# Kernel optimization log

Hardware: AMD Instinct MI355X
Metric: run time of the kernel (lower is better)

Reference implementation:

```python
import jax, jax.numpy as jnp
import numpy as np

BETA = 0.5   # mean-reversion rate of base drift
EPS = 1e-4   # guards T - t division at the final step


def setup_inputs() -> dict:
    key = jax.random.key(0)
    ks = jax.random.split(key, 8)
    B, DX, DW, H, NS = 1024, 32, 32, 128, 500
    ts = jnp.arange(NS + 1, dtype=jnp.float32) / NS  # uniform grid on [0, 1]
    return {
        "x0": jax.random.normal(ks[0], (B, DX), jnp.float32),
        "ts": ts,
        "dWs": jax.random.normal(ks[1], (NS, B, DW), jnp.float32),
        "W1": jax.random.normal(ks[2], (DX + 1, H), jnp.float32) / np.sqrt(DX + 1),
        "b1": jnp.zeros((H,), jnp.float32),
        "W2": jax.random.normal(ks[3], (H, H), jnp.float32) / np.sqrt(H),
        "b2": jnp.zeros((H,), jnp.float32),
        "W3": jax.random.normal(ks[4], (H, DW), jnp.float32) / np.sqrt(H),
        "b3": jnp.zeros((DW,), jnp.float32),
        "Gmat": 0.3 * jax.random.normal(ks[5], (DX, DW), jnp.float32),
        "mu": jax.random.normal(ks[6], (DX,), jnp.float32),
        "v_target": jax.random.normal(ks[7], (DX,), jnp.float32),
    }


def reference(x0, ts, dWs, W1, b1, W2, b2, W3, b3, Gmat, mu, v_target):
    T = ts[-1]
    dts = jnp.diff(ts)                                   # [NS]
    dW_scaled = dWs * jnp.sqrt(dts)[:, None, None]       # [NS, B, DW]
    a = Gmat @ Gmat.T                                    # diffusion covariance [DX, DX]

    def mlp(t, x):  # x: [B, DX] -> [B, DW]
        inp = jnp.concatenate([jnp.full((x.shape[0], 1), t, x.dtype), x], axis=-1)
        h = jnp.tanh(inp @ W1 + b1)
        h = jnp.tanh(h @ W2 + b2)
        return h @ W3 + b3

    def scan_body(carry, vals):
        t, x, ll = carry
        dt, dW = vals
        r = (v_target - x) / (T - t + EPS)               # guided score r_tilde
        f_base = BETA * (mu - x)
        f_circ = f_base + r @ a                          # a symmetric: a @ r per batch row
        v = mlp(t, x)                                    # nn(t, x)
        drift = f_circ + v @ Gmat.T                      # f + g @ nn_output
        x_new = x + drift * dt + dW @ Gmat.T             # Euler-Maruyama step
        Gval = jnp.einsum('bd,bd->b', f_base, r) - 0.5 * jnp.einsum('bd,bd->b', r, r @ a)
        ll_new = ll + Gval * dt
        return (t + dt, x_new, ll_new), (x_new, v)

    init = (ts[0], x0, jnp.zeros(x0.shape[0], x0.dtype))
    (_, _, ll), (xs, vs) = jax.lax.scan(scan_body, init, (dts, dW_scaled))
    return xs, vs, ll
```

## Files before the change

kernel.cpp:

```cpp
#include <hip/hip_runtime.h>
#include <math.h>

#define NSTEPS 500
#define BATCH  1024
#define DX     32
#define DW     32
#define HDIM   128
#define BETA   0.5f
#define EPSG   1e-4f
#define SC     2.8853900817779268f

typedef short bf8_t __attribute__((ext_vector_type(8)));
typedef float f4_t  __attribute__((ext_vector_type(4)));

union U8 { bf8_t v; unsigned u[4]; };

__device__ __forceinline__ f4_t MFMA(bf8_t a, bf8_t b, f4_t c) {
    return __builtin_amdgcn_mfma_f32_16x16x32_bf16(a, b, c, 0, 0, 0);
}

__device__ __forceinline__ unsigned short f2bf(float x) {
    unsigned u = __float_as_uint(x);
    u += 0x7fffu + ((u >> 16) & 1u);
    return (unsigned short)(u >> 16);
}
__device__ __forceinline__ float bf2f(unsigned short h) {
    return __uint_as_float(((unsigned)h) << 16);
}
__device__ __forceinline__ unsigned cvtpk(float a, float b) {
    unsigned r;
    asm("v_cvt_pk_bf16_f32 %0, %1, %2" : "=v"(r) : "v"(a), "v"(b));
    return r;
}
__device__ __forceinline__ float unplo(unsigned u) { return __uint_as_float(u << 16); }
__device__ __forceinline__ float unphi(unsigned u) { return __uint_as_float(u & 0xffff0000u); }

__device__ __forceinline__ float exp2_hw(float x) {
    float r; asm("v_exp_f32 %0, %1" : "=v"(r) : "v"(x)); return r;
}
__device__ __forceinline__ float rcp_hw(float x) {
    float r; asm("v_rcp_f32 %0, %1" : "=v"(r) : "v"(x)); return r;
}
__device__ __forceinline__ float sigm_s(float zs) {
    return rcp_hw(exp2_hw(zs) + 1.f);
}
__device__ __forceinline__ void hilo_pk(float a, float b, unsigned& hp, unsigned& lp) {
    hp = cvtpk(a, b);
    lp = cvtpk(a - unplo(hp), b - unphi(hp));
}
__device__ __forceinline__ void agpr_pin(bf8_t& v) { asm("" : "+a"(v)); }

__device__ __forceinline__ void bar_lds() {
    __builtin_amdgcn_sched_barrier(0);
    asm volatile("s_waitcnt lgkmcnt(0)" ::: "memory");
    __builtin_amdgcn_s_barrier();
    __builtin_amdgcn_sched_barrier(0);
}

__global__ __launch_bounds__(256, 1)
void sde_kernel(const float* __restrict__ x0, const float* __restrict__ ts,
                const float* __restrict__ dWs,
                const float* __restrict__ W1, const float* __restrict__ b1,
                const float* __restrict__ W2, const float* __restrict__ b2,
                const float* __restrict__ W3, const float* __restrict__ b3,
                const float* __restrict__ G,  const float* __restrict__ mu,
                const float* __restrict__ vt, float* __restrict__ out)
{
    __shared__ float sts[NSTEPS + 1];
    __shared__ __align__(16) float sG[DX * DW];
    __shared__ __align__(16) unsigned sH1[4][64][4];
    __shared__ __align__(16) unsigned sB2[4][64][4];
    __shared__ __align__(16) unsigned sUH[2][64][2];
    __shared__ __align__(16) unsigned sUL[2][64][2];
    __shared__ __align__(16) f4_t sRA[2][64];
    __shared__ float sLL[2][16];

    const int tid  = threadIdx.x;
    const int w    = tid >> 6;
    const int lane = tid & 63;
    const int m16  = lane & 15;
    const int quad = lane >> 4;
    const int r0   = blockIdx.x * 16;
    const int brow = r0 + m16;

    for (int i = tid; i <= NSTEPS; i += 256) sts[i] = ts[i];
    for (int i = tid; i < DX * DW; i += 256) sG[i] = G[i];
    __syncthreads();

    int foS[8], ktG[4];
    #pragma unroll
    for (int j = 0; j < 8; ++j) foS[j] = (j < 4) ? (4 * quad + j) : (16 + 4 * quad + (j - 4));
    #pragma unroll
    for (int kf = 0; kf < 4; ++kf) ktG[kf] = (w + kf) & 3;

    bf8_t w1a[2];
    #pragma unroll
    for (int ml = 0; ml < 2; ++ml) {
        int mtg = 2 * w + ml;
        #pragma unroll
        for (int j = 0; j < 8; ++j)
            w1a[ml][j] = (short)f2bf(SC * W1[(1 + foS[j]) * HDIM + mtg * 16 + m16]);
        agpr_pin(w1a[ml]);
    }
    bf8_t w2a[2][4];
    #pragma unroll
    for (int ml = 0; ml < 2; ++ml) {
        int mtg = 2 * w + ml;
        #pragma unroll
        for (int kf = 0; kf < 4; ++kf) {
            #pragma unroll
            for (int j = 0; j < 8; ++j)
                w2a[ml][kf][j] = (short)f2bf(-2.f * SC * W2[(ktG[kf] * 32 + foS[j]) * HDIM + mtg * 16 + m16]);
            agpr_pin(w2a[ml][kf]);
        }
    }

    bf8_t ones;
    #pragma unroll
    for (int j = 0; j < 8; ++j) ones[j] = (short)0x3f80;

    f4_t b2C[2];
    #pragma unroll
    for (int ml = 0; ml < 2; ++ml) {
        f4_t S = {0, 0, 0, 0};
        #pragma unroll
        for (int kf = 0; kf < 4; ++kf) S = MFMA(w2a[ml][kf], ones, S);
        #pragma unroll
        for (int i = 0; i < 4; ++i)
            b2C[ml][i] = fmaf(-0.5f, S[i], SC * b2[(2 * w + ml) * 16 + 4 * quad + i]);
    }

    f4_t cin[2];
    unsigned w10p[4];
    {
        float t0 = ts[0];
        #pragma unroll
        for (int ml = 0; ml < 2; ++ml) {
            int f0 = (2 * w + ml) * 16 + 4 * quad;
            float wa = SC * W1[f0],     wb = SC * W1[f0 + 1];
            float wc = SC * W1[f0 + 2], wd = SC * W1[f0 + 3];
            w10p[2 * ml]     = ((unsigned)f2bf(wb) << 16) | f2bf(wa);
            w10p[2 * ml + 1] = ((unsigned)f2bf(wd) << 16) | f2bf(wc);
            cin[ml][0] = fmaf(t0, wa, SC * b1[f0]);
            cin[ml][1] = fmaf(t0, wb, SC * b1[f0 + 1]);
            cin[ml][2] = fmaf(t0, wc, SC * b1[f0 + 2]);
            cin[ml][3] = fmaf(t0, wd, SC * b1[f0 + 3]);
        }
    }

    f4_t bmu[2];
    float vtr[2][4];
    #pragma unroll
    for (int mt = 0; mt < 2; ++mt)
        #pragma unroll
        for (int i = 0; i < 4; ++i) {
            int f = mt * 16 + 4 * quad + i;
            bmu[mt][i] = BETA * mu[f];
            vtr[mt][i] = vt[f];
        }

    bf8_t ghi[2], glo[2];
    #pragma unroll
    for (int mt = 0; mt < 2; ++mt) {
        #pragma unroll
        for (int j = 0; j < 8; ++j) {
            float gv = sG[(mt * 16 + m16) * DW + foS[j]];
            unsigned short hg = f2bf(gv);
            ghi[mt][j] = (short)hg;
            glo[mt][j] = (short)f2bf(gv - bf2f(hg));
        }
        agpr_pin(ghi[mt]); agpr_pin(glo[mt]);
    }

    bf8_t w3a[4], ahi, alo;
    f4_t b3C, cw;
    if (w < 2) {
        #pragma unroll
        for (int kf = 0; kf < 4; ++kf) {
            #pragma unroll
            for (int j = 0; j < 8; ++j)
                w3a[kf][j] = (short)f2bf(-2.f * W3[(ktG[kf] * 32 + foS[j]) * DW + w * 16 + m16]);
            agpr_pin(w3a[kf]);
        }
        f4_t S = {0, 0, 0, 0};
        #pragma unroll
        for (int kf = 0; kf < 4; ++kf) S = MFMA(w3a[kf], ones, S);
        #pragma unroll
        for (int i = 0; i < 4; ++i)
            b3C[i] = fmaf(-0.5f, S[i], b3[w * 16 + 4 * quad + i]);
        cw = ((const f4_t*)(dWs + (size_t)brow * DW))[w * 4 + quad];
    } else {
        int rowA = (w - 2) * 16 + m16;
        float gb[32];
        const f4_t* pb = (const f4_t*)(sG + rowA * DW);
        #pragma unroll
        for (int k4 = 0; k4 < 8; ++k4) {
            f4_t t = pb[k4];
            gb[4 * k4] = t[0]; gb[4 * k4 + 1] = t[1]; gb[4 * k4 + 2] = t[2]; gb[4 * k4 + 3] = t[3];
        }
        #pragma unroll
        for (int j = 0; j < 8; ++j) {
            const f4_t* pa = (const f4_t*)(sG + foS[j] * DW);
            float acc = 0.f;
            #pragma unroll
            for (int k4 = 0; k4 < 8; ++k4) {
                f4_t t = pa[k4];
                acc += t[0] * gb[4 * k4] + t[1] * gb[4 * k4 + 1]
                     + t[2] * gb[4 * k4 + 2] + t[3] * gb[4 * k4 + 3];
            }
            unsigned short h = f2bf(acc);
            ahi[j] = (short)h;
            alo[j] = (short)f2bf(acc - bf2f(h));
        }
        agpr_pin(ahi); agpr_pin(alo);
    }

    f4_t xr[2];
    {
        const f4_t* p = (const f4_t*)(x0 + (size_t)brow * DX);
        xr[0] = p[quad]; xr[1] = p[4 + quad];
    }

    const float T = sts[NSTEPS];
    float tcur = sts[0];
    float llr = 0.f;

    float* xs_out = out;
    float* vs_out = out + (size_t)NSTEPS * BATCH * DX;
    float* ll_out = out + (size_t)2 * NSTEPS * BATCH * DX;

    #pragma unroll 1
    for (int s = 0; s < NSTEPS; ++s) {
        const float tnx    = sts[s + 1];
        const float dt     = tnx - tcur;
        const float sqdt   = __builtin_amdgcn_sqrtf(dt);
        const float invrem = rcp_hw(T - tcur + EPSG);

        f4_t nw;
        if (w < 2) {
            int sn = (s + 1 < NSTEPS) ? s + 1 : s;
            nw = ((const f4_t*)(dWs + (size_t)sn * (BATCH * DW) + (size_t)brow * DW))[w * 4 + quad];
        }

        U8 xb;
        xb.u[0] = cvtpk(xr[0][0], xr[0][1]); xb.u[1] = cvtpk(xr[0][2], xr[0][3]);
        xb.u[2] = cvtpk(xr[1][0], xr[1][1]); xb.u[3] = cvtpk(xr[1][2], xr[1][3]);
        U8 bhO;
        #pragma unroll
        for (int ml = 0; ml < 2; ++ml) {
            f4_t acc = MFMA(w1a[ml], xb.v, cin[ml]);
            bhO.u[2 * ml]     = cvtpk(sigm_s(acc[0]), sigm_s(acc[1]));
            bhO.u[2 * ml + 1] = cvtpk(sigm_s(acc[2]), sigm_s(acc[3]));
        }
        *(uint4*)&sH1[w][lane][0] = make_uint4(bhO.u[0], bhO.u[1], bhO.u[2], bhO.u[3]);

        float rr[2][4];
        f4_t raO;
        if (w >= 2) {
            #pragma unroll
            for (int mt = 0; mt < 2; ++mt)
                #pragma unroll
                for (int i = 0; i < 4; ++i) rr[mt][i] = (vtr[mt][i] - xr[mt][i]) * invrem;
            U8 rh, rl;
            hilo_pk(rr[0][0], rr[0][1], rh.u[0], rl.u[0]);
            hilo_pk(rr[0][2], rr[0][3], rh.u[1], rl.u[1]);
            hilo_pk(rr[1][0], rr[1][1], rh.u[2], rl.u[2]);
            hilo_pk(rr[1][2], rr[1][3], rh.u[3], rl.u[3]);
            raO = f4_t{0, 0, 0, 0};
            raO = MFMA(ahi, rh.v, raO);
            raO = MFMA(ahi, rl.v, raO);
            raO = MFMA(alo, rh.v, raO);
        }
        bar_lds();

        uint4 h1 = *(const uint4*)&sH1[ktG[1]][lane][0];
        uint4 h2 = *(const uint4*)&sH1[ktG[2]][lane][0];
        uint4 h3 = *(const uint4*)&sH1[ktG[3]][lane][0];
        U8 f1, f2, f3;
        f1.u[0] = h1.x; f1.u[1] = h1.y; f1.u[2] = h1.z; f1.u[3] = h1.w;
        f2.u[0] = h2.x; f2.u[1] = h2.y; f2.u[2] = h2.z; f2.u[3] = h2.w;
        f3.u[0] = h3.x; f3.u[1] = h3.y; f3.u[2] = h3.z; f3.u[3] = h3.w;
        U8 b2O;
        #pragma unroll
        for (int ml = 0; ml < 2; ++ml) {
            f4_t acc = b2C[ml];
            acc = MFMA(w2a[ml][0], bhO.v, acc);
            acc = MFMA(w2a[ml][1], f1.v, acc);
            acc = MFMA(w2a[ml][2], f2.v, acc);
            acc = MFMA(w2a[ml][3], f3.v, acc);
            b2O.u[2 * ml]     = cvtpk(sigm_s(acc[0]), sigm_s(acc[1]));
            b2O.u[2 * ml + 1] = cvtpk(sigm_s(acc[2]), sigm_s(acc[3]));
        }
        *(uint4*)&sB2[w][lane][0] = make_uint4(b2O.u[0], b2O.u[1], b2O.u[2], b2O.u[3]);
        bar_lds();

        f4_t vA;
        if (w < 2) {
            uint4 p1 = *(const uint4*)&sB2[ktG[1]][lane][0];
            uint4 p2 = *(const uint4*)&sB2[ktG[2]][lane][0];
            uint4 p3 = *(const uint4*)&sB2[ktG[3]][lane][0];
            U8 g1, g2, g3;
            g1.u[0] = p1.x; g1.u[1] = p1.y; g1.u[2] = p1.z; g1.u[3] = p1.w;
            g2.u[0] = p2.x; g2.u[1] = p2.y; g2.u[2] = p2.z; g2.u[3] = p2.w;
            g3.u[0] = p3.x; g3.u[1] = p3.y; g3.u[2] = p3.z; g3.u[3] = p3.w;
            vA = b3C;
            vA = MFMA(w3a[0], b2O.v, vA);
            vA = MFMA(w3a[1], g1.v, vA);
            vA = MFMA(w3a[2], g2.v, vA);
            vA = MFMA(w3a[3], g3.v, vA);
            float u0 = fmaf(vA[0], dt, cw[0] * sqdt);
            float u1 = fmaf(vA[1], dt, cw[1] * sqdt);
            float u2 = fmaf(vA[2], dt, cw[2] * sqdt);
            float u3 = fmaf(vA[3], dt, cw[3] * sqdt);
            unsigned uh0, uh1, ul0, ul1;
            hilo_pk(u0, u1, uh0, ul0);
            hilo_pk(u2, u3, uh1, ul1);
            *(uint2*)&sUH[w][lane][0] = make_uint2(uh0, uh1);
            *(uint2*)&sUL[w][lane][0] = make_uint2(ul0, ul1);
        } else {
            sRA[w - 2][lane] = raO;
            int tw = w - 2;
            float gs = 0.f;
            #pragma unroll
            for (int i = 0; i < 4; ++i) {
                float fb = fmaf(-BETA, xr[tw][i], bmu[tw][i]);
                gs = fmaf(fb, rr[tw][i], gs);
                gs = fmaf(-0.5f * rr[tw][i], raO[i], gs);
            }
            llr = fmaf(gs, dt, llr);
        }
        bar_lds();

        uint2 ua = *(const uint2*)&sUH[0][lane][0];
        uint2 ub = *(const uint2*)&sUH[1][lane][0];
        uint2 la = *(const uint2*)&sUL[0][lane][0];
        uint2 lb = *(const uint2*)&sUL[1][lane][0];
        U8 uhF, ulF;
        uhF.u[0] = ua.x; uhF.u[1] = ua.y; uhF.u[2] = ub.x; uhF.u[3] = ub.y;
        ulF.u[0] = la.x; ulF.u[1] = la.y; ulF.u[2] = lb.x; ulF.u[3] = lb.y;
        f4_t raF0 = sRA[0][lane];
        f4_t raF1 = sRA[1][lane];
        f4_t xg0 = {0, 0, 0, 0}, xg1 = {0, 0, 0, 0};
        xg0 = MFMA(ghi[0], uhF.v, xg0);
        xg0 = MFMA(ghi[0], ulF.v, xg0);
        xg0 = MFMA(glo[0], uhF.v, xg0);
        xg1 = MFMA(ghi[1], uhF.v, xg1);
        xg1 = MFMA(ghi[1], ulF.v, xg1);
        xg1 = MFMA(glo[1], uhF.v, xg1);
        f4_t xo0, xo1;
        #pragma unroll
        for (int i = 0; i < 4; ++i) {
            float fb0 = fmaf(-BETA, xr[0][i], bmu[0][i]);
            float fb1 = fmaf(-BETA, xr[1][i], bmu[1][i]);
            xo0[i] = fmaf(fb0 + raF0[i], dt, xr[0][i]) + xg0[i];
            xo1[i] = fmaf(fb1 + raF1[i], dt, xr[1][i]) + xg1[i];
        }
        xr[0] = xo0; xr[1] = xo1;
        if (w < 2) {
            ((f4_t*)(xs_out + (size_t)s * (BATCH * DX) + (size_t)brow * DX))[w * 4 + quad] = (w == 0) ? xo0 : xo1;
            ((f4_t*)(vs_out + (size_t)s * (BATCH * DX) + (size_t)brow * DX))[w * 4 + quad] = vA;
            cw = nw;
        }

        #pragma unroll
        for (int ml = 0; ml < 2; ++ml) {
            unsigned wa = w10p[2 * ml], wb = w10p[2 * ml + 1];
            cin[ml][0] = fmaf(dt, unplo(wa), cin[ml][0]);
            cin[ml][1] = fmaf(dt, unphi(wa), cin[ml][1]);
            cin[ml][2] = fmaf(dt, unplo(wb), cin[ml][2]);
            cin[ml][3] = fmaf(dt, unphi(wb), cin[ml][3]);
        }
        tcur = tnx;
    }

    if (w >= 2) {
        llr += __shfl_xor(llr, 16, 64);
        llr += __shfl_xor(llr, 32, 64);
        if (lane < 16) sLL[w - 2][lane] = llr;
    }
    bar_lds();
    if (w == 0 && lane < 16) ll_out[r0 + lane] = sLL[0][lane] + sLL[1][lane];
}

extern "C" void kernel_launch(void* const* d_in, const int* in_sizes, int n_in,
                              void* d_out, int out_size, void* d_ws, size_t ws_size,
                              hipStream_t stream) {
    const float* x0 = (const float*)d_in[0];
    const float* ts = (const float*)d_in[1];
    const float* dWs = (const float*)d_in[2];
    const float* W1 = (const float*)d_in[3];
    const float* b1 = (const float*)d_in[4];
    const float* W2 = (const float*)d_in[5];
    const float* b2 = (const float*)d_in[6];
    const float* W3 = (const float*)d_in[7];
    const float* b3 = (const float*)d_in[8];
    const float* G  = (const float*)d_in[9];
    const float* mu = (const float*)d_in[10];
    const float* vt = (const float*)d_in[11];
    hipLaunchKernelGGL(sde_kernel, dim3(BATCH / 16), dim3(256), 0, stream,
                       x0, ts, dWs, W1, b1, W2, b2, W3, b3, G, mu, vt, (float*)d_out);
}
```

Measured before the change: 816.2 us.

## Process two 16-row batch tiles per workgroup to interleave independent MFMA chains

Each workgroup now handles 32 batch rows as two independent 16-row tiles (A and B) and issues their MFMA chains together, so the latency of one serial chain can be hidden behind the other. The grid is halved to 32 blocks, which leaves many MI355X compute units idle in a sequential 500-step loop but halves the number of barriers per row. The change also adds a second s_barrier inside bar_lds, which looks accidental and adds synchronisation cost. Register pressure roughly doubles for the per-row state, which may cause spills under launch_bounds(256,1).

```diff
diff --git a/kernel.cpp b/kernel.cpp
--- a/kernel.cpp
+++ b/kernel.cpp
@@ -53,6 +53,7 @@
 __device__ __forceinline__ void bar_lds() {
     __builtin_amdgcn_sched_barrier(0);
     asm volatile("s_waitcnt lgkmcnt(0)" ::: "memory");
+    __builtin_amdgcn_s_barrier();
     __builtin_amdgcn_s_barrier();
     __builtin_amdgcn_sched_barrier(0);
 }
@@ -68,20 +69,21 @@
 {
     __shared__ float sts[NSTEPS + 1];
     __shared__ __align__(16) float sG[DX * DW];
-    __shared__ __align__(16) unsigned sH1[4][64][4];
-    __shared__ __align__(16) unsigned sB2[4][64][4];
-    __shared__ __align__(16) unsigned sUH[2][64][2];
-    __shared__ __align__(16) unsigned sUL[2][64][2];
-    __shared__ __align__(16) f4_t sRA[2][64];
-    __shared__ float sLL[2][16];
+    __shared__ __align__(16) unsigned sH1[2][4][64][4];
+    __shared__ __align__(16) unsigned sB2[2][4][64][4];
+    __shared__ __align__(16) unsigned sUH[2][2][64][2];
+    __shared__ __align__(16) unsigned sUL[2][2][64][2];
+    __shared__ __align__(16) f4_t sRA[2][2][64];
+    __shared__ float sLL[2][2][16];
 
     const int tid  = threadIdx.x;
     const int w    = tid >> 6;
     const int lane = tid & 63;
     const int m16  = lane & 15;
     const int quad = lane >> 4;
-    const int r0   = blockIdx.x * 16;
-    const int brow = r0 + m16;
+    const int r0   = blockIdx.x * 32;
+    const int browA = r0 + m16;
+    const int browB = r0 + 16 + m16;
 
     for (int i = tid; i <= NSTEPS; i += 256) sts[i] = ts[i];
     for (int i = tid; i < DX * DW; i += 256) sG[i] = G[i];
@@ -173,7 +175,7 @@
     }
 
     bf8_t w3a[4], ahi, alo;
-    f4_t b3C, cw;
+    f4_t b3C, cwA, cwB;
     if (w < 2) {
         #pragma unroll
         for (int kf = 0; kf < 4; ++kf) {
@@ -188,7 +190,8 @@
         #pragma unroll
         for (int i = 0; i < 4; ++i)
             b3C[i] = fmaf(-0.5f, S[i], b3[w * 16 + 4 * quad + i]);
-        cw = ((const f4_t*)(dWs + (size_t)brow * DW))[w * 4 + quad];
+        cwA = ((const f4_t*)(dWs + (size_t)browA * DW))[w * 4 + quad];
+        cwB = ((const f4_t*)(dWs + (size_t)browB * DW))[w * 4 + quad];
     } else {
         int rowA = (w - 2) * 16 + m16;
         float gb[32];
@@ -215,15 +218,17 @@
         agpr_pin(ahi); agpr_pin(alo);
     }
 
-    f4_t xr[2];
+    f4_t xrA[2], xrB[2];
     {
-        const f4_t* p = (const f4_t*)(x0 + (size_t)brow * DX);
-        xr[0] = p[quad]; xr[1] = p[4 + quad];
+        const f4_t* pA = (const f4_t*)(x0 + (size_t)browA * DX);
+        const f4_t* pB = (const f4_t*)(x0 + (size_t)browB * DX);
+        xrA[0] = pA[quad]; xrA[1] = pA[4 + quad];
+        xrB[0] = pB[quad]; xrB[1] = pB[4 + quad];
     }
 
     const float T = sts[NSTEPS];
     float tcur = sts[0];
-    float llr = 0.f;
+    float llrA = 0.f, llrB = 0.f;
 
     float* xs_out = out;
     float* vs_out = out + (size_t)NSTEPS * BATCH * DX;
@@ -236,130 +241,213 @@
         const float sqdt   = __builtin_amdgcn_sqrtf(dt);
         const float invrem = rcp_hw(T - tcur + EPSG);
 
-        f4_t nw;
+        f4_t nwA, nwB;
         if (w < 2) {
             int sn = (s + 1 < NSTEPS) ? s + 1 : s;
-            nw = ((const f4_t*)(dWs + (size_t)sn * (BATCH * DW) + (size_t)brow * DW))[w * 4 + quad];
-        }
-
-        U8 xb;
-        xb.u[0] = cvtpk(xr[0][0], xr[0][1]); xb.u[1] = cvtpk(xr[0][2], xr[0][3]);
-        xb.u[2] = cvtpk(xr[1][0], xr[1][1]); xb.u[3] = cvtpk(xr[1][2], xr[1][3]);
-        U8 bhO;
+            const float* base = dWs + (size_t)sn * (BATCH * DW);
+            nwA = ((const f4_t*)(base + (size_t)browA * DW))[w * 4 + quad];
+            nwB = ((const f4_t*)(base + (size_t)browB * DW))[w * 4 + quad];
+        }
+
+        U8 xbA, xbB;
+        xbA.u[0] = cvtpk(xrA[0][0], xrA[0][1]); xbA.u[1] = cvtpk(xrA[0][2], xrA[0][3]);
+        xbA.u[2] = cvtpk(xrA[1][0], xrA[1][1]); xbA.u[3] = cvtpk(xrA[1][2], xrA[1][3]);
+        xbB.u[0] = cvtpk(xrB[0][0], xrB[0][1]); xbB.u[1] = cvtpk(xrB[0][2], xrB[0][3]);
+        xbB.u[2] = cvtpk(xrB[1][0], xrB[1][1]); xbB.u[3] = cvtpk(xrB[1][2], xrB[1][3]);
+        U8 bhA, bhB;
         #pragma unroll
         for (int ml = 0; ml < 2; ++ml) {
-            f4_t acc = MFMA(w1a[ml], xb.v, cin[ml]);
-            bhO.u[2 * ml]     = cvtpk(sigm_s(acc[0]), sigm_s(acc[1]));
-            bhO.u[2 * ml + 1] = cvtpk(sigm_s(acc[2]), sigm_s(acc[3]));
-        }
-        *(uint4*)&sH1[w][lane][0] = make_uint4(bhO.u[0], bhO.u[1], bhO.u[2], bhO.u[3]);
-
-        float rr[2][4];
-        f4_t raO;
+            f4_t aA = MFMA(w1a[ml], xbA.v, cin[ml]);
+            f4_t aB = MFMA(w1a[ml], xbB.v, cin[ml]);
+            bhA.u[2 * ml]     = cvtpk(sigm_s(aA[0]), sigm_s(aA[1]));
+            bhA.u[2 * ml + 1] = cvtpk(sigm_s(aA[2]), sigm_s(aA[3]));
+            bhB.u[2 * ml]     = cvtpk(sigm_s(aB[0]), sigm_s(aB[1]));
+            bhB.u[2 * ml + 1] = cvtpk(sigm_s(aB[2]), sigm_s(aB[3]));
+        }
+        *(uint4*)&sH1[0][w][lane][0] = make_uint4(bhA.u[0], bhA.u[1], bhA.u[2], bhA.u[3]);
+        *(uint4*)&sH1[1][w][lane][0] = make_uint4(bhB.u[0], bhB.u[1], bhB.u[2], bhB.u[3]);
+
+        float rrA[2][4], rrB[2][4];
+        f4_t raA, raB;
         if (w >= 2) {
             #pragma unroll
             for (int mt = 0; mt < 2; ++mt)
                 #pragma unroll
-                for (int i = 0; i < 4; ++i) rr[mt][i] = (vtr[mt][i] - xr[mt][i]) * invrem;
-            U8 rh, rl;
-            hilo_pk(rr[0][0], rr[0][1], rh.u[0], rl.u[0]);
-            hilo_pk(rr[0][2], rr[0][3], rh.u[1], rl.u[1]);
-            hilo_pk(rr[1][0], rr[1][1], rh.u[2], rl.u[2]);
-            hilo_pk(rr[1][2], rr[1][3], rh.u[3], rl.u[3]);
-            raO = f4_t{0, 0, 0, 0};
-            raO = MFMA(ahi, rh.v, raO);
-            raO = MFMA(ahi, rl.v, raO);
-            raO = MFMA(alo, rh.v, raO);
+                for (int i = 0; i < 4; ++i) {
+                    rrA[mt][i] = (vtr[mt][i] - xrA[mt][i]) * invrem;
+                    rrB[mt][i] = (vtr[mt][i] - xrB[mt][i]) * invrem;
+                }
+            U8 rhA, rlA, rhB, rlB;
+            hilo_pk(rrA[0][0], rrA[0][1], rhA.u[0], rlA.u[0]);
+            hilo_pk(rrA[0][2], rrA[0][3], rhA.u[1], rlA.u[1]);
+            hilo_pk(rrA[1][0], rrA[1][1], rhA.u[2], rlA.u[2]);
+            hilo_pk(rrA[1][2], rrA[1][3], rhA.u[3], rlA.u[3]);
+            hilo_pk(rrB[0][0], rrB[0][1], rhB.u[0], rlB.u[0]);
+            hilo_pk(rrB[0][2], rrB[0][3], rhB.u[1], rlB.u[1]);
+            hilo_pk(rrB[1][0], rrB[1][1], rhB.u[2], rlB.u[2]);
+            hilo_pk(rrB[1][2], rrB[1][3], rhB.u[3], rlB.u[3]);
+            raA = f4_t{0, 0, 0, 0};
+            raA = MFMA(ahi, rhA.v, raA);
+            raA = MFMA(ahi, rlA.v, raA);
+            raA = MFMA(alo, rhA.v, raA);
+            raB = f4_t{0, 0, 0, 0};
+            raB = MFMA(ahi, rhB.v, raB);
+            raB = MFMA(ahi, rlB.v, raB);
+            raB = MFMA(alo, rhB.v, raB);
         }
         bar_lds();
 
-        uint4 h1 = *(const uint4*)&sH1[ktG[1]][lane][0];
-        uint4 h2 = *(const uint4*)&sH1[ktG[2]][lane][0];
-        uint4 h3 = *(const uint4*)&sH1[ktG[3]][lane][0];
-        U8 f1, f2, f3;
-        f1.u[0] = h1.x; f1.u[1] = h1.y; f1.u[2] = h1.z; f1.u[3] = h1.w;
-        f2.u[0] = h2.x; f2.u[1] = h2.y; f2.u[2] = h2.z; f2.u[3] = h2.w;
-        f3.u[0] = h3.x; f3.u[1] = h3.y; f3.u[2] = h3.z; f3.u[3] = h3.w;
-        U8 b2O;
+        uint4 a1 = *(const uint4*)&sH1[0][ktG[1]][lane][0];
+        uint4 a2 = *(const uint4*)&sH1[0][ktG[2]][lane][0];
+        uint4 a3 = *(const uint4*)&sH1[0][ktG[3]][lane][0];
+        uint4 c1 = *(const uint4*)&sH1[1][ktG[1]][lane][0];
+        uint4 c2 = *(const uint4*)&sH1[1][ktG[2]][lane][0];
+        uint4 c3 = *(const uint4*)&sH1[1][ktG[3]][lane][0];
+        U8 fA1, fA2, fA3, fB1, fB2, fB3;
+        fA1.u[0] = a1.x; fA1.u[1] = a1.y; fA1.u[2] = a1.z; fA1.u[3] = a1.w;
+        fA2.u[0] = a2.x; fA2.u[1] = a2.y; fA2.u[2] = a2.z; fA2.u[3] = a2.w;
+        fA3.u[0] = a3.x; fA3.u[1] = a3.y; fA3.u[2] = a3.z; fA3.u[3] = a3.w;
+        fB1.u[0] = c1.x; fB1.u[1] = c1.y; fB1.u[2] = c1.z; fB1.u[3] = c1.w;
+        fB2.u[0] = c2.x; fB2.u[1] = c2.y; fB2.u[2] = c2.z; fB2.u[3] = c2.w;
+        fB3.u[0] = c3.x; fB3.u[1] = c3.y; fB3.u[2] = c3.z; fB3.u[3] = c3.w;
+        U8 b2A, b2B;
         #pragma unroll
         for (int ml = 0; ml < 2; ++ml) {
-            f4_t acc = b2C[ml];
-            acc = MFMA(w2a[ml][0], bhO.v, acc);
-            acc = MFMA(w2a[ml][1], f1.v, acc);
-            acc = MFMA(w2a[ml][2], f2.v, acc);
-            acc = MFMA(w2a[ml][3], f3.v, acc);
-            b2O.u[2 * ml]     = cvtpk(sigm_s(acc[0]), sigm_s(acc[1]));
-            b2O.u[2 * ml + 1] = cvtpk(sigm_s(acc[2]), sigm_s(acc[3]));
-        }
-        *(uint4*)&sB2[w][lane][0] = make_uint4(b2O.u[0], b2O.u[1], b2O.u[2], b2O.u[3]);
+            f4_t aA = b2C[ml];
+            aA = MFMA(w2a[ml][0], bhA.v, aA);
+            aA = MFMA(w2a[ml][1], fA1.v, aA);
+            aA = MFMA(w2a[ml][2], fA2.v, aA);
+            aA = MFMA(w2a[ml][3], fA3.v, aA);
+            f4_t aB = b2C[ml];
+            aB = MFMA(w2a[ml][0], bhB.v, aB);
+            aB = MFMA(w2a[ml][1], fB1.v, aB);
+            aB = MFMA(w2a[ml][2], fB2.v, aB);
+            aB = MFMA(w2a[ml][3], fB3.v, aB);
+            b2A.u[2 * ml]     = cvtpk(sigm_s(aA[0]), sigm_s(aA[1]));
+            b2A.u[2 * ml + 1] = cvtpk(sigm_s(aA[2]), sigm_s(aA[3]));
+            b2B.u[2 * ml]     = cvtpk(sigm_s(aB[0]), sigm_s(aB[1]));
+            b2B.u[2 * ml + 1] = cvtpk(sigm_s(aB[2]), sigm_s(aB[3]));
+        }
+        *(uint4*)&sB2[0][w][lane][0] = make_uint4(b2A.u[0], b2A.u[1], b2A.u[2], b2A.u[3]);
+        *(uint4*)&sB2[1][w][lane][0] = make_uint4(b2B.u[0], b2B.u[1], b2B.u[2], b2B.u[3]);
         bar_lds();
 
-        f4_t vA;
+        f4_t vAA, vAB;
         if (w < 2) {
-            uint4 p1 = *(const uint4*)&sB2[ktG[1]][lane][0];
-            uint4 p2 = *(const uint4*)&sB2[ktG[2]][lane][0];
-            uint4 p3 = *(const uint4*)&sB2[ktG[3]][lane][0];
-            U8 g1, g2, g3;
-            g1.u[0] = p1.x; g1.u[1] = p1.y; g1.u[2] = p1.z; g1.u[3] = p1.w;
-            g2.u[0] = p2.x; g2.u[1] = p2.y; g2.u[2] = p2.z; g2.u[3] = p2.w;
-            g3.u[0] = p3.x; g3.u[1] = p3.y; g3.u[2] = p3.z; g3.u[3] = p3.w;
-            vA = b3C;
-            vA = MFMA(w3a[0], b2O.v, vA);
-            vA = MFMA(w3a[1], g1.v, vA);
-            vA = MFMA(w3a[2], g2.v, vA);
-            vA = MFMA(w3a[3], g3.v, vA);
-            float u0 = fmaf(vA[0], dt, cw[0] * sqdt);
-            float u1 = fmaf(vA[1], dt, cw[1] * sqdt);
-            float u2 = fmaf(vA[2], dt, cw[2] * sqdt);
-            float u3 = fmaf(vA[3], dt, cw[3] * sqdt);
-            unsigned uh0, uh1, ul0, ul1;
-            hilo_pk(u0, u1, uh0, ul0);
-            hilo_pk(u2, u3, uh1, ul1);
-            *(uint2*)&sUH[w][lane][0] = make_uint2(uh0, uh1);
-            *(uint2*)&sUL[w][lane][0] = make_uint2(ul0, ul1);
+            uint4 p1 = *(const uint4*)&sB2[0][ktG[1]][lane][0];
+            uint4 p2 = *(const uint4*)&sB2[0][ktG[2]][lane][0];
+            uint4 p3 = *(const uint4*)&sB2[0][ktG[3]][lane][0];
+            uint4 q1 = *(const uint4*)&sB2[1][ktG[1]][lane][0];
+            uint4 q2 = *(const uint4*)&sB2[1][ktG[2]][lane][0];
+            uint4 q3 = *(const uint4*)&sB2[1][ktG[3]][lane][0];
+            U8 gA1, gA2, gA3, gB1, gB2, gB3;
+            gA1.u[0] = p1.x; gA1.u[1] = p1.y; gA1.u[2] = p1.z; gA1.u[3] = p1.w;
+            gA2.u[0] = p2.x; gA2.u[1] = p2.y; gA2.u[2] = p2.z; gA2.u[3] = p2.w;
+            gA3.u[0] = p3.x; gA3.u[1] = p3.y; gA3.u[2] = p3.z; gA3.u[3] = p3.w;
+            gB1.u[0] = q1.x; gB1.u[1] = q1.y; gB1.u[2] = q1.z; gB1.u[3] = q1.w;
+            gB2.u[0] = q2.x; gB2.u[1] = q2.y; gB2.u[2] = q2.z; gB2.u[3] = q2.w;
+            gB3.u[0] = q3.x; gB3.u[1] = q3.y; gB3.u[2] = q3.z; gB3.u[3] = q3.w;
+            vAA = b3C;
+            vAA = MFMA(w3a[0], b2A.v, vAA);
+            vAA = MFMA(w3a[1], gA1.v, vAA);
+            vAA = MFMA(w3a[2], gA2.v, vAA);
+            vAA = MFMA(w3a[3], gA3.v, vAA);
+            vAB = b3C;
+            vAB = MFMA(w3a[0], b2B.v, vAB);
+            vAB = MFMA(w3a[1], gB1.v, vAB);
+            vAB = MFMA(w3a[2], gB2.v, vAB);
+            vAB = MFMA(w3a[3], gB3.v, vAB);
+            float uA0 = fmaf(vAA[0], dt, cwA[0] * sqdt);
+            float uA1 = fmaf(vAA[1], dt, cwA[1] * sqdt);
+            float uA2 = fmaf(vAA[2], dt, cwA[2] * sqdt);
+            float uA3 = fmaf(vAA[3], dt, cwA[3] * sqdt);
+            float uB0 = fmaf(vAB[0], dt, cwB[0] * sqdt);
+            float uB1 = fmaf(vAB[1], dt, cwB[1] * sqdt);
+            float uB2 = fmaf(vAB[2], dt, cwB[2] * sqdt);
+            float uB3 = fmaf(vAB[3], dt, cwB[3] * sqdt);
+            unsigned h0, h1, l0, l1;
+            hilo_pk(uA0, uA1, h0, l0);
+            hilo_pk(uA2, uA3, h1, l1);
+            *(uint2*)&sUH[0][w][lane][0] = make_uint2(h0, h1);
+            *(uint2*)&sUL[0][w][lane][0] = make_uint2(l0, l1);
+            hilo_pk(uB0, uB1, h0, l0);
+            hilo_pk(uB2, uB3, h1, l1);
+            *(uint2*)&sUH[1][w][lane][0] = make_uint2(h0, h1);
+            *(uint2*)&sUL[1][w][lane][0] = make_uint2(l0, l1);
         } else {
-            sRA[w - 2][lane] = raO;
+            sRA[0][w - 2][lane] = raA;
+            sRA[1][w - 2][lane] = raB;
             int tw = w - 2;
-            float gs = 0.f;
+            float gsA = 0.f, gsB = 0.f;
             #pragma unroll
             for (int i = 0; i < 4; ++i) {
-                float fb = fmaf(-BETA, xr[tw][i], bmu[tw][i]);
-                gs = fmaf(fb, rr[tw][i], gs);
-                gs = fmaf(-0.5f * rr[tw][i], raO[i], gs);
+                float fbA = fmaf(-BETA, xrA[tw][i], bmu[tw][i]);
+                float fbB = fmaf(-BETA, xrB[tw][i], bmu[tw][i]);
+                gsA = fmaf(fbA, rrA[tw][i], gsA);
+                gsA = fmaf(-0.5f * rrA[tw][i], raA[i], gsA);
+                gsB = fmaf(fbB, rrB[tw][i], gsB);
+                gsB = fmaf(-0.5f * rrB[tw][i], raB[i], gsB);
             }
-            llr = fmaf(gs, dt, llr);
+            llrA = fmaf(gsA, dt, llrA);
+            llrB = fmaf(gsB, dt, llrB);
         }
         bar_lds();
 
-        uint2 ua = *(const uint2*)&sUH[0][lane][0];
-        uint2 ub = *(const uint2*)&sUH[1][lane][0];
-        uint2 la = *(const uint2*)&sUL[0][lane][0];
-        uint2 lb = *(const uint2*)&sUL[1][lane][0];
-        U8 uhF, ulF;
-        uhF.u[0] = ua.x; uhF.u[1] = ua.y; uhF.u[2] = ub.x; uhF.u[3] = ub.y;
-        ulF.u[0] = la.x; ulF.u[1] = la.y; ulF.u[2] = lb.x; ulF.u[3] = lb.y;
-        f4_t raF0 = sRA[0][lane];
-        f4_t raF1 = sRA[1][lane];
-        f4_t xg0 = {0, 0, 0, 0}, xg1 = {0, 0, 0, 0};
-        xg0 = MFMA(ghi[0], uhF.v, xg0);
-        xg0 = MFMA(ghi[0], ulF.v, xg0);
-        xg0 = MFMA(glo[0], uhF.v, xg0);
-        xg1 = MFMA(ghi[1], uhF.v, xg1);
-        xg1 = MFMA(ghi[1], ulF.v, xg1);
-        xg1 = MFMA(glo[1], uhF.v, xg1);
-        f4_t xo0, xo1;
+        uint2 uaA = *(const uint2*)&sUH[0][0][lane][0];
+        uint2 ubA = *(const uint2*)&sUH[0][1][lane][0];
+        uint2 laA = *(const uint2*)&sUL[0][0][lane][0];
+        uint2 lbA = *(const uint2*)&sUL[0][1][lane][0];
+        uint2 uaB = *(const uint2*)&sUH[1][0][lane][0];
+        uint2 ubB = *(const uint2*)&sUH[1][1][lane][0];
+        uint2 laB = *(const uint2*)&sUL[1][0][lane][0];
+        uint2 lbB = *(const uint2*)&sUL[1][1][lane][0];
+        U8 uhA, ulA, uhB, ulB;
+        uhA.u[0] = uaA.x; uhA.u[1] = uaA.y; uhA.u[2] = ubA.x; uhA.u[3] = ubA.y;
+        ulA.u[0] = laA.x; ulA.u[1] = laA.y; ulA.u[2] = lbA.x; ulA.u[3] = lbA.y;
+        uhB.u[0] = uaB.x; uhB.u[1] = uaB.y; uhB.u[2] = ubB.x; uhB.u[3] = ubB.y;
+        ulB.u[0] = laB.x; ulB.u[1] = laB.y; ulB.u[2] = lbB.x; ulB.u[3] = lbB.y;
+        f4_t rA0 = sRA[0][0][lane];
+        f4_t rA1 = sRA[0][1][lane];
+        f4_t rB0 = sRA[1][0][lane];
+        f4_t rB1 = sRA[1][1][lane];
+        f4_t xgA0 = {0, 0, 0, 0}, xgA1 = {0, 0, 0, 0};
+        f4_t xgB0 = {0, 0, 0, 0}, xgB1 = {0, 0, 0, 0};
+        xgA0 = MFMA(ghi[0], uhA.v, xgA0);
+        xgA0 = MFMA(ghi[0], ulA.v, xgA0);
+        xgA0 = MFMA(glo[0], uhA.v, xgA0);
+        xgA1 = MFMA(ghi[1], uhA.v, xgA1);
+        xgA1 = MFMA(ghi[1], ulA.v, xgA1);
+        xgA1 = MFMA(glo[1], uhA.v, xgA1);
+        xgB0 = MFMA(ghi[0], uhB.v, xgB0);
+        xgB0 = MFMA(ghi[0], ulB.v, xgB0);
+        xgB0 = MFMA(glo[0], uhB.v, xgB0);
+        xgB1 = MFMA(ghi[1], uhB.v, xgB1);
+        xgB1 = MFMA(ghi[1], ulB.v, xgB1);
+        xgB1 = MFMA(glo[1], uhB.v, xgB1);
+        f4_t xoA0, xoA1, xoB0, xoB1;
         #pragma unroll
         for (int i = 0; i < 4; ++i) {
-            float fb0 = fmaf(-BETA, xr[0][i], bmu[0][i]);
-            float fb1 = fmaf(-BETA, xr[1][i], bmu[1][i]);
-            xo0[i] = fmaf(fb0 + raF0[i], dt, xr[0][i]) + xg0[i];
-            xo1[i] = fmaf(fb1 + raF1[i], dt, xr[1][i]) + xg1[i];
-        }
-        xr[0] = xo0; xr[1] = xo1;
+            float fbA0 = fmaf(-BETA, xrA[0][i], bmu[0][i]);
+            float fbA1 = fmaf(-BETA, xrA[1][i], bmu[1][i]);
+            float fbB0 = fmaf(-BETA, xrB[0][i], bmu[0][i]);
+            float fbB1 = fmaf(-BETA, xrB[1][i], bmu[1][i]);
+            xoA0[i] = fmaf(fbA0 + rA0[i], dt, xrA[0][i]) + xgA0[i];
+            xoA1[i] = fmaf(fbA1 + rA1[i], dt, xrA[1][i]) + xgA1[i];
+            xoB0[i] = fmaf(fbB0 + rB0[i], dt, xrB[0][i]) + xgB0[i];
+            xoB1[i] = fmaf(fbB1 + rB1[i], dt, xrB[1][i]) + xgB1[i];
+        }
+        xrA[0] = xoA0; xrA[1] = xoA1;
+        xrB[0] = xoB0; xrB[1] = xoB1;
         if (w < 2) {
-            ((f4_t*)(xs_out + (size_t)s * (BATCH * DX) + (size_t)brow * DX))[w * 4 + quad] = (w == 0) ? xo0 : xo1;
-            ((f4_t*)(vs_out + (size_t)s * (BATCH * DX) + (size_t)brow * DX))[w * 4 + quad] = vA;
-            cw = nw;
+            f4_t* pxA = (f4_t*)(xs_out + (size_t)s * (BATCH * DX) + (size_t)browA * DX);
+            f4_t* pxB = (f4_t*)(xs_out + (size_t)s * (BATCH * DX) + (size_t)browB * DX);
+            f4_t* pvA = (f4_t*)(vs_out + (size_t)s * (BATCH * DX) + (size_t)browA * DX);
+            f4_t* pvB = (f4_t*)(vs_out + (size_t)s * (BATCH * DX) + (size_t)browB * DX);
+            pxA[w * 4 + quad] = (w == 0) ? xoA0 : xoA1;
+            pxB[w * 4 + quad] = (w == 0) ? xoB0 : xoB1;
+            pvA[w * 4 + quad] = vAA;
+            pvB[w * 4 + quad] = vAB;
+            cwA = nwA; cwB = nwB;
         }
 
         #pragma unroll
@@ -374,12 +462,20 @@
     }
 
     if (w >= 2) {
-        llr += __shfl_xor(llr, 16, 64);
-        llr += __shfl_xor(llr, 32, 64);
-        if (lane < 16) sLL[w - 2][lane] = llr;
+        llrA += __shfl_xor(llrA, 16, 64);
+        llrA += __shfl_xor(llrA, 32, 64);
+        llrB += __shfl_xor(llrB, 16, 64);
+        llrB += __shfl_xor(llrB, 32, 64);
+        if (lane < 16) {
+            sLL[0][w - 2][lane] = llrA;
+            sLL[1][w - 2][lane] = llrB;
+        }
     }
     bar_lds();
-    if (w == 0 && lane < 16) ll_out[r0 + lane] = sLL[0][lane] + sLL[1][lane];
+    if (w == 0 && lane < 16) {
+        ll_out[r0 + lane]      = sLL[0][0][lane] + sLL[0][1][lane];
+        ll_out[r0 + 16 + lane] = sLL[1][0][lane] + sLL[1][1][lane];
+    }
 }
 
 extern "C" void kernel_launch(void* const* d_in, const int* in_sizes, int n_in,
@@ -397,6 +493,6 @@
     const float* G  = (const float*)d_in[9];
     const float* mu = (const float*)d_in[10];
     const float* vt = (const float*)d_in[11];
-    hipLaunchKernelGGL(sde_kernel, dim3(BATCH / 16), dim3(256), 0, stream,
+    hipLaunchKernelGGL(sde_kernel, dim3(BATCH / 32), dim3(256), 0, stream,
                        x0, ts, dWs, W1, b1, W2, b2, W3, b3, G, mu, vt, (float*)d_out);
 }
```

Result: slower. 1.056 ms (+29.4%).

## Replicate layer-3 and state update in every wave to drop a barrier

Applied to the files above, without the earlier changes.

Every wave now computes the full W3 output, the r·a product and the G·u update redundantly, so the third LDS exchange (sUH/sUL/sRA) and its barrier per step disappear. The per-step critical path loses one barrier and LDS round trip. In exchange each wave carries more MFMAs and more AGPR-pinned weights, and output stores are spread across the four waves. The log-likelihood reduction now happens within a single wave.

```diff
diff --git a/kernel.cpp b/kernel.cpp
--- a/kernel.cpp
+++ b/kernel.cpp
@@ -70,10 +70,6 @@
     __shared__ __align__(16) float sG[DX * DW];
     __shared__ __align__(16) unsigned sH1[4][64][4];
     __shared__ __align__(16) unsigned sB2[4][64][4];
-    __shared__ __align__(16) unsigned sUH[2][64][2];
-    __shared__ __align__(16) unsigned sUL[2][64][2];
-    __shared__ __align__(16) f4_t sRA[2][64];
-    __shared__ float sLL[2][16];
 
     const int tid  = threadIdx.x;
     const int w    = tid >> 6;
@@ -114,6 +110,16 @@
             agpr_pin(w2a[ml][kf]);
         }
     }
+    bf8_t w3a[2][4];
+    #pragma unroll
+    for (int mt = 0; mt < 2; ++mt)
+        #pragma unroll
+        for (int kf = 0; kf < 4; ++kf) {
+            #pragma unroll
+            for (int j = 0; j < 8; ++j)
+                w3a[mt][kf][j] = (short)f2bf(-2.f * W3[(ktG[kf] * 32 + foS[j]) * DW + mt * 16 + m16]);
+            agpr_pin(w3a[mt][kf]);
+        }
 
     bf8_t ones;
     #pragma unroll
@@ -128,6 +134,16 @@
         #pragma unroll
         for (int i = 0; i < 4; ++i)
             b2C[ml][i] = fmaf(-0.5f, S[i], SC * b2[(2 * w + ml) * 16 + 4 * quad + i]);
+    }
+    f4_t b3C[2];
+    #pragma unroll
+    for (int mt = 0; mt < 2; ++mt) {
+        f4_t S = {0, 0, 0, 0};
+        #pragma unroll
+        for (int kf = 0; kf < 4; ++kf) S = MFMA(w3a[mt][kf], ones, S);
+        #pragma unroll
+        for (int i = 0; i < 4; ++i)
+            b3C[mt][i] = fmaf(-0.5f, S[i], b3[mt * 16 + 4 * quad + i]);
     }
 
     f4_t cin[2];
@@ -159,38 +175,10 @@
             vtr[mt][i] = vt[f];
         }
 
-    bf8_t ghi[2], glo[2];
+    bf8_t ghi[2], glo[2], ahi[2], alo[2];
     #pragma unroll
     for (int mt = 0; mt < 2; ++mt) {
-        #pragma unroll
-        for (int j = 0; j < 8; ++j) {
-            float gv = sG[(mt * 16 + m16) * DW + foS[j]];
-            unsigned short hg = f2bf(gv);
-            ghi[mt][j] = (short)hg;
-            glo[mt][j] = (short)f2bf(gv - bf2f(hg));
-        }
-        agpr_pin(ghi[mt]); agpr_pin(glo[mt]);
-    }
-
-    bf8_t w3a[4], ahi, alo;
-    f4_t b3C, cw;
-    if (w < 2) {
-        #pragma unroll
-        for (int kf = 0; kf < 4; ++kf) {
-            #pragma unroll
-            for (int j = 0; j < 8; ++j)
-                w3a[kf][j] = (short)f2bf(-2.f * W3[(ktG[kf] * 32 + foS[j]) * DW + w * 16 + m16]);
-            agpr_pin(w3a[kf]);
-        }
-        f4_t S = {0, 0, 0, 0};
-        #pragma unroll
-        for (int kf = 0; kf < 4; ++kf) S = MFMA(w3a[kf], ones, S);
-        #pragma unroll
-        for (int i = 0; i < 4; ++i)
-            b3C[i] = fmaf(-0.5f, S[i], b3[w * 16 + 4 * quad + i]);
-        cw = ((const f4_t*)(dWs + (size_t)brow * DW))[w * 4 + quad];
-    } else {
-        int rowA = (w - 2) * 16 + m16;
+        int rowA = mt * 16 + m16;
         float gb[32];
         const f4_t* pb = (const f4_t*)(sG + rowA * DW);
         #pragma unroll
@@ -209,10 +197,15 @@
                      + t[2] * gb[4 * k4 + 2] + t[3] * gb[4 * k4 + 3];
             }
             unsigned short h = f2bf(acc);
-            ahi[j] = (short)h;
-            alo[j] = (short)f2bf(acc - bf2f(h));
-        }
-        agpr_pin(ahi); agpr_pin(alo);
+            ahi[mt][j] = (short)h;
+            alo[mt][j] = (short)f2bf(acc - bf2f(h));
+            float gv = sG[rowA * DW + foS[j]];
+            unsigned short hg = f2bf(gv);
+            ghi[mt][j] = (short)hg;
+            glo[mt][j] = (short)f2bf(gv - bf2f(hg));
+        }
+        agpr_pin(ghi[mt]); agpr_pin(glo[mt]);
+        agpr_pin(ahi[mt]); agpr_pin(alo[mt]);
     }
 
     f4_t xr[2];
@@ -220,6 +213,11 @@
         const f4_t* p = (const f4_t*)(x0 + (size_t)brow * DX);
         xr[0] = p[quad]; xr[1] = p[4 + quad];
     }
+    f4_t cw0, cw1;
+    {
+        const f4_t* p = (const f4_t*)(dWs + (size_t)brow * DW);
+        cw0 = p[quad]; cw1 = p[4 + quad];
+    }
 
     const float T = sts[NSTEPS];
     float tcur = sts[0];
@@ -228,6 +226,8 @@
     float* xs_out = out;
     float* vs_out = out + (size_t)NSTEPS * BATCH * DX;
     float* ll_out = out + (size_t)2 * NSTEPS * BATCH * DX;
+
+    const int g1 = (w + 1) & 3, g2 = (w + 2) & 3, g3 = (w + 3) & 3;
 
     #pragma unroll 1
     for (int s = 0; s < NSTEPS; ++s) {
@@ -236,11 +236,33 @@
         const float sqdt   = __builtin_amdgcn_sqrtf(dt);
         const float invrem = rcp_hw(T - tcur + EPSG);
 
-        f4_t nw;
-        if (w < 2) {
+        f4_t nw0, nw1;
+        {
             int sn = (s + 1 < NSTEPS) ? s + 1 : s;
-            nw = ((const f4_t*)(dWs + (size_t)sn * (BATCH * DW) + (size_t)brow * DW))[w * 4 + quad];
-        }
+            const f4_t* p = (const f4_t*)(dWs + (size_t)sn * (BATCH * DW) + (size_t)brow * DW);
+            nw0 = p[quad]; nw1 = p[4 + quad];
+        }
+
+        float rr[2][4], fb[2][4];
+        #pragma unroll
+        for (int mt = 0; mt < 2; ++mt)
+            #pragma unroll
+            for (int i = 0; i < 4; ++i) {
+                rr[mt][i] = (vtr[mt][i] - xr[mt][i]) * invrem;
+                fb[mt][i] = fmaf(-BETA, xr[mt][i], bmu[mt][i]);
+            }
+        U8 rh, rl;
+        hilo_pk(rr[0][0], rr[0][1], rh.u[0], rl.u[0]);
+        hilo_pk(rr[0][2], rr[0][3], rh.u[1], rl.u[1]);
+        hilo_pk(rr[1][0], rr[1][1], rh.u[2], rl.u[2]);
+        hilo_pk(rr[1][2], rr[1][3], rh.u[3], rl.u[3]);
+        f4_t ra0 = {0, 0, 0, 0}, ra1 = {0, 0, 0, 0};
+        ra0 = MFMA(ahi[0], rh.v, ra0);
+        ra0 = MFMA(ahi[0], rl.v, ra0);
+        ra0 = MFMA(alo[0], rh.v, ra0);
+        ra1 = MFMA(ahi[1], rh.v, ra1);
+        ra1 = MFMA(ahi[1], rl.v, ra1);
+        ra1 = MFMA(alo[1], rh.v, ra1);
 
         U8 xb;
         xb.u[0] = cvtpk(xr[0][0], xr[0][1]); xb.u[1] = cvtpk(xr[0][2], xr[0][3]);
@@ -253,33 +275,26 @@
             bhO.u[2 * ml + 1] = cvtpk(sigm_s(acc[2]), sigm_s(acc[3]));
         }
         *(uint4*)&sH1[w][lane][0] = make_uint4(bhO.u[0], bhO.u[1], bhO.u[2], bhO.u[3]);
-
-        float rr[2][4];
-        f4_t raO;
-        if (w >= 2) {
+        bar_lds();
+
+        uint4 t1 = *(const uint4*)&sH1[g1][lane][0];
+        uint4 t2 = *(const uint4*)&sH1[g2][lane][0];
+        uint4 t3 = *(const uint4*)&sH1[g3][lane][0];
+        {
+            float gs = 0.f;
             #pragma unroll
-            for (int mt = 0; mt < 2; ++mt)
-                #pragma unroll
-                for (int i = 0; i < 4; ++i) rr[mt][i] = (vtr[mt][i] - xr[mt][i]) * invrem;
-            U8 rh, rl;
-            hilo_pk(rr[0][0], rr[0][1], rh.u[0], rl.u[0]);
-            hilo_pk(rr[0][2], rr[0][3], rh.u[1], rl.u[1]);
-            hilo_pk(rr[1][0], rr[1][1], rh.u[2], rl.u[2]);
-            hilo_pk(rr[1][2], rr[1][3], rh.u[3], rl.u[3]);
-            raO = f4_t{0, 0, 0, 0};
-            raO = MFMA(ahi, rh.v, raO);
-            raO = MFMA(ahi, rl.v, raO);
-            raO = MFMA(alo, rh.v, raO);
-        }
-        bar_lds();
-
-        uint4 h1 = *(const uint4*)&sH1[ktG[1]][lane][0];
-        uint4 h2 = *(const uint4*)&sH1[ktG[2]][lane][0];
-        uint4 h3 = *(const uint4*)&sH1[ktG[3]][lane][0];
+            for (int i = 0; i < 4; ++i) {
+                gs = fmaf(fb[0][i], rr[0][i], gs);
+                gs = fmaf(-0.5f * rr[0][i], ra0[i], gs);
+                gs = fmaf(fb[1][i], rr[1][i], gs);
+                gs = fmaf(-0.5f * rr[1][i], ra1[i], gs);
+            }
+            llr = fmaf(gs, dt, llr);
+        }
         U8 f1, f2, f3;
-        f1.u[0] = h1.x; f1.u[1] = h1.y; f1.u[2] = h1.z; f1.u[3] = h1.w;
-        f2.u[0] = h2.x; f2.u[1] = h2.y; f2.u[2] = h2.z; f2.u[3] = h2.w;
-        f3.u[0] = h3.x; f3.u[1] = h3.y; f3.u[2] = h3.z; f3.u[3] = h3.w;
+        f1.u[0] = t1.x; f1.u[1] = t1.y; f1.u[2] = t1.z; f1.u[3] = t1.w;
+        f2.u[0] = t2.x; f2.u[1] = t2.y; f2.u[2] = t2.z; f2.u[3] = t2.w;
+        f3.u[0] = t3.x; f3.u[1] = t3.y; f3.u[2] = t3.z; f3.u[3] = t3.w;
         U8 b2O;
         #pragma unroll
         for (int ml = 0; ml < 2; ++ml) {
@@ -294,74 +309,12 @@
         *(uint4*)&sB2[w][lane][0] = make_uint4(b2O.u[0], b2O.u[1], b2O.u[2], b2O.u[3]);
         bar_lds();
 
-        f4_t vA;
-        if (w < 2) {
-            uint4 p1 = *(const uint4*)&sB2[ktG[1]][lane][0];
-            uint4 p2 = *(const uint4*)&sB2[ktG[2]][lane][0];
-            uint4 p3 = *(const uint4*)&sB2[ktG[3]][lane][0];
-            U8 g1, g2, g3;
-            g1.u[0] = p1.x; g1.u[1] = p1.y; g1.u[2] = p1.z; g1.u[3] = p1.w;
-            g2.u[0] = p2.x; g2.u[1] = p2.y; g2.u[2] = p2.z; g2.u[3] = p2.w;
-            g3.u[0] = p3.x; g3.u[1] = p3.y; g3.u[2] = p3.z; g3.u[3] = p3.w;
-            vA = b3C;
-            vA = MFMA(w3a[0], b2O.v, vA);
-            vA = MFMA(w3a[1], g1.v, vA);
-            vA = MFMA(w3a[2], g2.v, vA);
-            vA = MFMA(w3a[3], g3.v, vA);
-            float u0 = fmaf(vA[0], dt, cw[0] * sqdt);
-            float u1 = fmaf(vA[1], dt, cw[1] * sqdt);
-            float u2 = fmaf(vA[2], dt, cw[2] * sqdt);
-            float u3 = fmaf(vA[3], dt, cw[3] * sqdt);
-            unsigned uh0, uh1, ul0, ul1;
-            hilo_pk(u0, u1, uh0, ul0);
-            hilo_pk(u2, u3, uh1, ul1);
-            *(uint2*)&sUH[w][lane][0] = make_uint2(uh0, uh1);
-            *(uint2*)&sUL[w][lane][0] = make_uint2(ul0, ul1);
-        } else {
-            sRA[w - 2][lane] = raO;
-            int tw = w - 2;
-            float gs = 0.f;
-            #pragma unroll
-            for (int i = 0; i < 4; ++i) {
-                float fb = fmaf(-BETA, xr[tw][i], bmu[tw][i]);
-                gs = fmaf(fb, rr[tw][i], gs);
-                gs = fmaf(-0.5f * rr[tw][i], raO[i], gs);
-            }
-            llr = fmaf(gs, dt, llr);
-        }
-        bar_lds();
-
-        uint2 ua = *(const uint2*)&sUH[0][lane][0];
-        uint2 ub = *(const uint2*)&sUH[1][lane][0];
-        uint2 la = *(const uint2*)&sUL[0][lane][0];
-        uint2 lb = *(const uint2*)&sUL[1][lane][0];
-        U8 uhF, ulF;
-        uhF.u[0] = ua.x; uhF.u[1] = ua.y; uhF.u[2] = ub.x; uhF.u[3] = ub.y;
-        ulF.u[0] = la.x; ulF.u[1] = la.y; ulF.u[2] = lb.x; ulF.u[3] = lb.y;
-        f4_t raF0 = sRA[0][lane];
-        f4_t raF1 = sRA[1][lane];
-        f4_t xg0 = {0, 0, 0, 0}, xg1 = {0, 0, 0, 0};
-        xg0 = MFMA(ghi[0], uhF.v, xg0);
-        xg0 = MFMA(ghi[0], ulF.v, xg0);
-        xg0 = MFMA(glo[0], uhF.v, xg0);
-        xg1 = MFMA(ghi[1], uhF.v, xg1);
-        xg1 = MFMA(ghi[1], ulF.v, xg1);
-        xg1 = MFMA(glo[1], uhF.v, xg1);
-        f4_t xo0, xo1;
-        #pragma unroll
-        for (int i = 0; i < 4; ++i) {
-            float fb0 = fmaf(-BETA, xr[0][i], bmu[0][i]);
-            float fb1 = fmaf(-BETA, xr[1][i], bmu[1][i]);
-            xo0[i] = fmaf(fb0 + raF0[i], dt, xr[0][i]) + xg0[i];
-            xo1[i] = fmaf(fb1 + raF1[i], dt, xr[1][i]) + xg1[i];
-        }
-        xr[0] = xo0; xr[1] = xo1;
-        if (w < 2) {
-            ((f4_t*)(xs_out + (size_t)s * (BATCH * DX) + (size_t)brow * DX))[w * 4 + quad] = (w == 0) ? xo0 : xo1;
-            ((f4_t*)(vs_out + (size_t)s * (BATCH * DX) + (size_t)brow * DX))[w * 4 + quad] = vA;
-            cw = nw;
-        }
-
+        uint4 p1 = *(const uint4*)&sB2[g1][lane][0];
+        uint4 p2 = *(const uint4*)&sB2[g2][lane][0];
+        uint4 p3 = *(const uint4*)&sB2[g3][lane][0];
+        f4_t dws0, dws1;
+        #pragma unroll
+        for (int i = 0; i < 4; ++i) { dws0[i] = cw0[i] * sqdt; dws1[i] = cw1[i] * sqdt; }
         #pragma unroll
         for (int ml = 0; ml < 2; ++ml) {
             unsigned wa = w10p[2 * ml], wb = w10p[2 * ml + 1];
@@ -370,16 +323,65 @@
             cin[ml][2] = fmaf(dt, unplo(wb), cin[ml][2]);
             cin[ml][3] = fmaf(dt, unphi(wb), cin[ml][3]);
         }
+        U8 q1, q2, q3;
+        q1.u[0] = p1.x; q1.u[1] = p1.y; q1.u[2] = p1.z; q1.u[3] = p1.w;
+        q2.u[0] = p2.x; q2.u[1] = p2.y; q2.u[2] = p2.z; q2.u[3] = p2.w;
+        q3.u[0] = p3.x; q3.u[1] = p3.y; q3.u[2] = p3.z; q3.u[3] = p3.w;
+        f4_t v0a = b3C[0], v1a = b3C[1];
+        v0a = MFMA(w3a[0][0], b2O.v, v0a);
+        v1a = MFMA(w3a[1][0], b2O.v, v1a);
+        v0a = MFMA(w3a[0][1], q1.v, v0a);
+        v1a = MFMA(w3a[1][1], q1.v, v1a);
+        v0a = MFMA(w3a[0][2], q2.v, v0a);
+        v1a = MFMA(w3a[1][2], q2.v, v1a);
+        v0a = MFMA(w3a[0][3], q3.v, v0a);
+        v1a = MFMA(w3a[1][3], q3.v, v1a);
+
+        float u_[2][4];
+        #pragma unroll
+        for (int i = 0; i < 4; ++i) {
+            u_[0][i] = fmaf(v0a[i], dt, dws0[i]);
+            u_[1][i] = fmaf(v1a[i], dt, dws1[i]);
+        }
+        U8 uh, ul;
+        hilo_pk(u_[0][0], u_[0][1], uh.u[0], ul.u[0]);
+        hilo_pk(u_[0][2], u_[0][3], uh.u[1], ul.u[1]);
+        hilo_pk(u_[1][0], u_[1][1], uh.u[2], ul.u[2]);
+        hilo_pk(u_[1][2], u_[1][3], uh.u[3], ul.u[3]);
+        f4_t xg0 = {0, 0, 0, 0}, xg1 = {0, 0, 0, 0};
+        xg0 = MFMA(ghi[0], uh.v, xg0);
+        xg1 = MFMA(ghi[1], uh.v, xg1);
+        xg0 = MFMA(ghi[0], ul.v, xg0);
+        xg1 = MFMA(ghi[1], ul.v, xg1);
+        xg0 = MFMA(glo[0], uh.v, xg0);
+        xg1 = MFMA(glo[1], uh.v, xg1);
+
+        f4_t xo0, xo1;
+        #pragma unroll
+        for (int i = 0; i < 4; ++i) {
+            xo0[i] = fmaf(fb[0][i] + ra0[i], dt, xr[0][i]) + xg0[i];
+            xo1[i] = fmaf(fb[1][i] + ra1[i], dt, xr[1][i]) + xg1[i];
+        }
+        xr[0] = xo0; xr[1] = xo1;
+
+        {
+            float* xbase = xs_out + (size_t)s * (BATCH * DX) + (size_t)brow * DX;
+            float* vbase = vs_out + (size_t)s * (BATCH * DX) + (size_t)brow * DX;
+            if (w == 0)      ((f4_t*)xbase)[quad]     = xo0;
+            else if (w == 1) ((f4_t*)xbase)[4 + quad] = xo1;
+            else if (w == 2) ((f4_t*)vbase)[quad]     = v0a;
+            else             ((f4_t*)vbase)[4 + quad] = v1a;
+        }
+
+        cw0 = nw0; cw1 = nw1;
         tcur = tnx;
     }
 
-    if (w >= 2) {
+    if (w == 0) {
         llr += __shfl_xor(llr, 16, 64);
         llr += __shfl_xor(llr, 32, 64);
-        if (lane < 16) sLL[w - 2][lane] = llr;
-    }
-    bar_lds();
-    if (w == 0 && lane < 16) ll_out[r0 + lane] = sLL[0][lane] + sLL[1][lane];
+        if (lane < 16) ll_out[r0 + lane] = llr;
+    }
 }
 
 extern "C" void kernel_launch(void* const* d_in, const int* in_sizes, int n_in,
```

Measured after the change: 726.7 us. 11.0% less time.
